# Optimization experiments

Measured on AMD Instinct MI355X. Metric: run time of the kernel, lower is better.

Reference implementation:

```python
import jax, jax.numpy as jnp
import numpy as np
from functools import partial

D_MODEL = 1024
D_STATE = 16
D_CONV = 4
EXPAND = 2
DIM = EXPAND * D_MODEL  # 2048


def setup_inputs() -> dict:
    key = jax.random.key(0)
    ks = jax.random.split(key, 10)
    s = lambda fan_in: 1.0 / np.sqrt(fan_in)
    inp = {
        "x": jax.random.normal(ks[0], (8, 2048, D_MODEL), dtype=jnp.float32),
        "W_in": jax.random.normal(ks[1], (DIM, D_MODEL), dtype=jnp.float32) * s(D_MODEL),
        "b_in": jnp.zeros((DIM,), dtype=jnp.float32),
        "conv_w": jax.random.normal(ks[2], (DIM, 1, D_CONV), dtype=jnp.float32) * s(D_CONV),
        "conv_b": jnp.zeros((DIM,), dtype=jnp.float32),
        "W_x": jax.random.normal(ks[3], (3 * D_STATE, DIM), dtype=jnp.float32) * s(DIM),
        "W_dt": jax.random.normal(ks[4], (DIM, D_STATE), dtype=jnp.float32) * s(D_STATE),
        "b_dt": jnp.zeros((DIM,), dtype=jnp.float32),
        "W_out": jax.random.normal(ks[5], (D_MODEL, DIM), dtype=jnp.float32) * s(DIM),
        "b_out": jnp.zeros((D_MODEL,), dtype=jnp.float32),
    }
    return inp


def _selective_scan(xc, delta, A, Bm, Cm):
    # xc, delta: (B, L, DIM); Bm, Cm: (B, L, N); A: (N,)
    Bsz = xc.shape[0]
    h0 = jnp.zeros((Bsz, DIM, D_STATE), dtype=xc.dtype)

    def step(h, inputs):
        xc_t, d_t, b_t, c_t = inputs  # (B,DIM),(B,DIM),(B,N),(B,N)
        h = h * jnp.exp(d_t[:, :, None] * A) + xc_t[:, :, None] * b_t[:, None, :]
        y_t = jnp.einsum("bdn,bn->bd", h, c_t)
        return h, y_t

    tm = lambda a: jnp.swapaxes(a, 0, 1)  # time-major
    _, ys = jax.lax.scan(step, h0, (tm(xc), tm(delta), tm(Bm), tm(Cm)))
    return jnp.swapaxes(ys, 0, 1)  # (B, L, DIM)


def reference(x, W_in, b_in, conv_w, conv_b, W_x, W_dt, b_dt, W_out, b_out):
    A = -jnp.exp(jnp.linspace(0.0, -5.0, D_STATE).astype(x.dtype))  # (N,)
    xp = x @ W_in.T + b_in  # (B, L, DIM)
    # depthwise conv1d, padding=D_CONV-1 on BOTH sides (as torch Conv1d) -> length L+D_CONV-1
    xc = jax.lax.conv_general_dilated(
        jnp.swapaxes(xp, 1, 2), conv_w,
        window_strides=(1,), padding=[(D_CONV - 1, D_CONV - 1)],
        feature_group_count=DIM,
        dimension_numbers=("NCH", "OIH", "NCH"),
    ) + conv_b[None, :, None]
    xc = jnp.swapaxes(xc, 1, 2)  # (B, Lc, DIM)
    x_dbl = xc @ W_x.T  # (B, Lc, 3N)
    d_raw, Bm, Cm = jnp.split(x_dbl, [D_STATE, 2 * D_STATE], axis=-1)
    delta = jax.nn.softplus(d_raw @ W_dt.T + b_dt)  # (B, Lc, DIM)
    y = _selective_scan(xc, delta, A, Bm, Cm)  # (B, Lc, DIM)
    return y @ W_out.T + b_out  # (B, Lc, D_MODEL)
```

## Files before the change

### kernel.cpp

```cpp
#include <hip/hip_runtime.h>
#include <cstdint>
#include <cstddef>

#define B8 8
#define LSEQ 2048
#define LC 2051
#define DMODEL 1024
#define DIM 2048
#define LPAD 2054
#define M2 16408
#define M2P 16512
#define CS 32
#define NCH 65

typedef __attribute__((ext_vector_type(8))) short short8;
typedef __attribute__((ext_vector_type(4))) float floatx4;
typedef __attribute__((ext_vector_type(2))) float float2v;

__device__ __constant__ float AeT[16] = {
  -1.0f,          -0.71653131f, -0.51341712f, -0.36787944f,
  -0.26359714f,   -0.18887560f, -0.13533528f, -0.09697208f,
  -0.06948345f,   -0.04978707f, -0.03567399f, -0.02556154f,
  -0.01831564f,   -0.01312373f, -0.00940356f, -0.00673795f};

#define LOG2E 1.44269504088896f

__device__ __forceinline__ float bf2f(unsigned short h) {
  union { unsigned int u; float f; } v; v.u = ((unsigned int)h) << 16; return v.f;
}
__device__ __forceinline__ unsigned short f2bf(float f) {
  union { float f; unsigned int u; } v; v.f = f;
  unsigned int r = (v.u + 0x7FFFu + ((v.u >> 16) & 1u)) >> 16;
  return (unsigned short)r;
}

__device__ __forceinline__ float2v pk_mul_vv(float2v a, float2v b) {
  float2v d; asm("v_pk_mul_f32 %0, %1, %2" : "=v"(d) : "v"(a), "v"(b)); return d;
}
__device__ __forceinline__ float2v pk_mul_sv(float2v bs, float2v a) {
  float2v d; asm("v_pk_mul_f32 %0, %1, %2" : "=v"(d) : "s"(bs), "v"(a)); return d;
}
__device__ __forceinline__ float2v pk_fma_vvv(float2v a, float2v b, float2v c) {
  float2v d; asm("v_pk_fma_f32 %0, %1, %2, %3" : "=v"(d) : "v"(a), "v"(b), "v"(c)); return d;
}
__device__ __forceinline__ float2v pk_fma_vsv(float2v a, float2v bs, float2v c) {
  float2v d; asm("v_pk_fma_f32 %0, %1, %2, %3" : "=v"(d) : "v"(a), "s"(bs), "v"(c)); return d;
}
__device__ __forceinline__ float2v pk_add_vv(float2v a, float2v b) {
  float2v d; asm("v_pk_add_f32 %0, %1, %2" : "=v"(d) : "v"(a), "v"(b)); return d;
}
__device__ __forceinline__ float exp2_raw(float x) {
  float d; asm("v_exp_f32 %0, %1" : "=v"(d) : "v"(x)); return d;
}

__global__ __launch_bounds__(256) void cvt_f32_bf16(const float* __restrict__ in,
                                                    unsigned short* __restrict__ out,
                                                    int n8) {
  int i = blockIdx.x * 256 + threadIdx.x;
  if (i >= n8) return;
  const float4* p = (const float4*)in + (size_t)i * 2;
  float4 a = p[0], b = p[1];
  uint4 o;
  o.x = (unsigned)f2bf(a.x) | ((unsigned)f2bf(a.y) << 16);
  o.y = (unsigned)f2bf(a.z) | ((unsigned)f2bf(a.w) << 16);
  o.z = (unsigned)f2bf(b.x) | ((unsigned)f2bf(b.y) << 16);
  o.w = (unsigned)f2bf(b.z) | ((unsigned)f2bf(b.w) << 16);
  *((uint4*)out + i) = o;
}

__global__ __launch_bounds__(256) void zero_pads(unsigned short* __restrict__ xp) {
  int i = blockIdx.x * 256 + threadIdx.x;
  int b = i / 1536;
  int r6 = (i % 1536) / 256;
  int dd = (i % 256) * 8;
  int row = (r6 < 3) ? r6 : (2048 + r6);
  uint4 z = make_uint4(0, 0, 0, 0);
  *(uint4*)(xp + ((size_t)b * LPAD + row) * DIM + dd) = z;
}

__global__ __launch_bounds__(256) void conv_kernel(const unsigned short* __restrict__ xp,
                                                   const float* __restrict__ conv_w,
                                                   const float* __restrict__ conv_b,
                                                   unsigned short* __restrict__ xc) {
  const int tc0 = blockIdx.x * 16;
  const int b = blockIdx.y;
  const int d0 = threadIdx.x * 8;

  float4 cw[8];
#pragma unroll
  for (int j = 0; j < 8; ++j) cw[j] = *(const float4*)(conv_w + (size_t)(d0 + j) * 4);
  float cb[8];
  {
    const float4* cb4 = (const float4*)(conv_b + d0);
    float4 c0 = cb4[0], c1 = cb4[1];
    cb[0] = c0.x; cb[1] = c0.y; cb[2] = c0.z; cb[3] = c0.w;
    cb[4] = c1.x; cb[5] = c1.y; cb[6] = c1.z; cb[7] = c1.w;
  }

  const unsigned short* base = xp + ((size_t)b * LPAD + tc0) * DIM + d0;
  unsigned short* outp = xc + ((size_t)b * LC + tc0) * DIM + d0;

  auto loadrow = [&](float (&w)[8], int r) {
    uint4 v = *(const uint4*)(base + (size_t)r * DIM);
    w[0] = bf2f(v.x & 0xffff); w[1] = bf2f(v.x >> 16);
    w[2] = bf2f(v.y & 0xffff); w[3] = bf2f(v.y >> 16);
    w[4] = bf2f(v.z & 0xffff); w[5] = bf2f(v.z >> 16);
    w[6] = bf2f(v.w & 0xffff); w[7] = bf2f(v.w >> 16);
  };

  float wa[8], wb[8], wc[8];
  loadrow(wa, 0); loadrow(wb, 1); loadrow(wc, 2);
#pragma unroll
  for (int i = 0; i < 16; ++i) {
    float wd[8];
    loadrow(wd, i + 3);
    if (tc0 + i < LC) {
      float acc[8];
#pragma unroll
      for (int j = 0; j < 8; ++j) {
        acc[j] = cb[j];
        acc[j] = fmaf(wa[j], cw[j].x, acc[j]);
        acc[j] = fmaf(wb[j], cw[j].y, acc[j]);
        acc[j] = fmaf(wc[j], cw[j].z, acc[j]);
        acc[j] = fmaf(wd[j], cw[j].w, acc[j]);
      }
      uint4 o;
      o.x = (unsigned)f2bf(acc[0]) | ((unsigned)f2bf(acc[1]) << 16);
      o.y = (unsigned)f2bf(acc[2]) | ((unsigned)f2bf(acc[3]) << 16);
      o.z = (unsigned)f2bf(acc[4]) | ((unsigned)f2bf(acc[5]) << 16);
      o.w = (unsigned)f2bf(acc[6]) | ((unsigned)f2bf(acc[7]) << 16);
      *(uint4*)(outp + (size_t)i * DIM) = o;
    }
#pragma unroll
    for (int j = 0; j < 8; ++j) { wa[j] = wb[j]; wb[j] = wc[j]; wc[j] = wd[j]; }
  }
}

#define GAS(p) ((const __attribute__((address_space(1))) void*)(p))
#define LAS(p) ((__attribute__((address_space(3))) void*)(p))

template <int MODE, int NBM, int NBN, int LX, int TAIL>
__global__ __launch_bounds__(256) void gemm_bt(const unsigned short* __restrict__ A,
                                               const unsigned short* __restrict__ Bw,
                                               const float* __restrict__ bias,
                                               void* __restrict__ Cout, int K) {
  const int gid = blockIdx.x;
  const int mainBlocks = 8 * LX * NBN;
  int bm, bn;
  if (TAIL && gid >= mainBlocks) {
    const int e = gid - mainBlocks;
    bm = 8 * LX + e / NBN;
    bn = e % NBN;
  } else {
    const int xcd = gid & 7;
    const int j = gid >> 3;
    bm = xcd * LX + (j % LX);
    bn = j / LX;
  }
  if (bm >= NBM) return;

  __shared__ __align__(16) unsigned short As[128 * 64];
  __shared__ __align__(16) unsigned short Bs[128 * 64];
  const int tid = threadIdx.x;
  const int lane = tid & 63, wave = tid >> 6;
  const int wr = wave >> 1, wc = wave & 1;

  floatx4 acc[4][4];
#pragma unroll
  for (int i = 0; i < 4; ++i)
#pragma unroll
    for (int j2 = 0; j2 < 4; ++j2) acc[i][j2] = (floatx4){0.f, 0.f, 0.f, 0.f};

  const int srow = tid >> 3;
  const int scol = ((tid & 7) ^ ((tid >> 3) & 7)) * 8;
  const unsigned short* Ab[4];
  const unsigned short* Bb[4];
#pragma unroll
  for (int L = 0; L < 4; ++L) {
    Ab[L] = A  + (size_t)(bm * 128 + L * 32 + srow) * K + scol;
    Bb[L] = Bw + (size_t)(bn * 128 + L * 32 + srow) * K + scol;
  }

  const int fr = lane & 15;
  const int hi = lane >> 4;
  const int fx = fr & 7;

  for (int k0 = 0; k0 < K; k0 += 64) {
    __syncthreads();
#pragma unroll
    for (int L = 0; L < 4; ++L) {
      __builtin_amdgcn_global_load_lds(GAS(Ab[L] + k0), LAS(As + L * 2048 + tid * 8), 16, 0, 0);
      __builtin_amdgcn_global_load_lds(GAS(Bb[L] + k0), LAS(Bs + L * 2048 + tid * 8), 16, 0, 0);
    }
    __syncthreads();

#pragma unroll
    for (int kk = 0; kk < 2; ++kk) {
      const int pb = ((kk * 4 + hi) ^ fx) * 8;
      short8 af[4], bf[4];
#pragma unroll
      for (int mt = 0; mt < 4; ++mt) af[mt] = *(const short8*)&As[(wr * 64 + mt * 16 + fr) * 64 + pb];
#pragma unroll
      for (int nt = 0; nt < 4; ++nt) bf[nt] = *(const short8*)&Bs[(wc * 64 + nt * 16 + fr) * 64 + pb];
#pragma unroll
      for (int mt = 0; mt < 4; ++mt)
#pragma unroll
        for (int nt = 0; nt < 4; ++nt)
          acc[mt][nt] = __builtin_amdgcn_mfma_f32_16x16x32_bf16(af[mt], bf[nt], acc[mt][nt], 0, 0, 0);
    }
  }

  const int er = (lane >> 4) * 4, ec = lane & 15;
#pragma unroll
  for (int mt = 0; mt < 4; ++mt) {
#pragma unroll
    for (int nt = 0; nt < 4; ++nt) {
#pragma unroll
      for (int i = 0; i < 4; ++i) {
        int r = bm * 128 + wr * 64 + mt * 16 + er + i;
        int c = bn * 128 + wc * 64 + nt * 16 + ec;
        float v = acc[mt][nt][i];
        if constexpr (MODE == 0) {
          int bb = r >> 11, t = r & 2047;
          ((unsigned short*)Cout)[((size_t)bb * LPAD + 3 + t) * DIM + c] = f2bf(v + bias[c]);
        } else if constexpr (MODE == 1) {
          if (r < M2 && c < 48) ((float*)Cout)[(size_t)r * 48 + c] = v;
        } else {
          if (r < M2) ((float*)Cout)[(size_t)r * DMODEL + c] = v + bias[c];
        }
      }
    }
  }
}

__global__ __launch_bounds__(256) void delta_kernel(const float* __restrict__ xdbl,
                                                    const float* __restrict__ W_dt,
                                                    const float* __restrict__ b_dt,
                                                    unsigned short* __restrict__ delta) {
  const int d = blockIdx.y * 256 + threadIdx.x;
  const int r0 = blockIdx.x * 8;
  float wv[16];
  const float4* wp = (const float4*)(W_dt + (size_t)d * 16);
#pragma unroll
  for (int q = 0; q < 4; ++q) {
    float4 t = wp[q];
    wv[q * 4 + 0] = t.x; wv[q * 4 + 1] = t.y; wv[q * 4 + 2] = t.z; wv[q * 4 + 3] = t.w;
  }
  const float bd = b_dt[d];
#pragma unroll
  for (int j = 0; j < 8; ++j) {
    const float* dr = xdbl + (size_t)(r0 + j) * 48;
    float z0 = bd, z1 = 0.f, z2 = 0.f, z3 = 0.f;
#pragma unroll
    for (int n = 0; n < 16; n += 4) {
      z0 = fmaf(dr[n + 0], wv[n + 0], z0);
      z1 = fmaf(dr[n + 1], wv[n + 1], z1);
      z2 = fmaf(dr[n + 2], wv[n + 2], z2);
      z3 = fmaf(dr[n + 3], wv[n + 3], z3);
    }
    float z = (z0 + z1) + (z2 + z3);
    float dl = (z > 20.f) ? z : __logf(1.f + __expf(z));
    delta[(size_t)(r0 + j) * DIM + d] = f2bf(dl);
  }
}

__global__ __launch_bounds__(256) void scan_pass1(const unsigned short* __restrict__ xc,
                                                  const unsigned short* __restrict__ dl,
                                                  const float* __restrict__ xd,
                                                  unsigned short* __restrict__ sdbuf,
                                                  unsigned short* __restrict__ qbuf) {
  const int wid = __builtin_amdgcn_readfirstlane((int)(threadIdx.x >> 6));
  const int lane = threadIdx.x & 63;
  const int W = blockIdx.x * 4 + wid;
  const int dg = W & 31;
  const int rest = W >> 5;
  const int c = rest % NCH;
  const int b = rest / NCH;
  const int d = dg * 64 + lane;
  const int t0 = c * CS;
  const int nst = (t0 + CS <= LC) ? CS : (LC - t0);

  float2v A2L[8];
#pragma unroll
  for (int i = 0; i < 8; ++i)
    A2L[i] = (float2v){AeT[2 * i] * LOG2E, AeT[2 * i + 1] * LOG2E};

  float2v h2[8];
#pragma unroll
  for (int i = 0; i < 8; ++i) h2[i] = (float2v){0.f, 0.f};
  float sumd = 0.f;

  const size_t row0 = (size_t)b * LC + t0;
  const float* xdb = xd + row0 * 48 + 16;
  const unsigned short* xcp = xc + row0 * DIM + d;
  const unsigned short* dp  = dl + row0 * DIM + d;

  auto body = [&](int s) {
    float2v Bv[8];
#pragma unroll
    for (int j = 0; j < 8; ++j) Bv[j] = *(const float2v*)(xdb + (size_t)s * 48 + 2 * j);
    float dlt = bf2f(dp[(size_t)s * DIM]);
    float xcv = bf2f(xcp[(size_t)s * DIM]);
    sumd += dlt;
    float2v dlt2 = (float2v){dlt, dlt};
    float2v xcv2 = (float2v){xcv, xcv};
#pragma unroll
    for (int i = 0; i < 8; ++i) {
      float2v arg = pk_mul_vv(dlt2, A2L[i]);
      float e0 = exp2_raw(arg.x), e1 = exp2_raw(arg.y);
      float2v e2 = (float2v){e0, e1};
      h2[i] = pk_fma_vvv(h2[i], e2, pk_mul_sv(Bv[i], xcv2));
    }
  };

  if (nst == CS) {
#pragma unroll
    for (int s = 0; s < CS; ++s) body(s);
  } else {
    for (int s = 0; s < nst; ++s) body(s);
  }

  sdbuf[((size_t)(b * NCH + c) << 11) + d] = f2bf(sumd);
  const size_t base = ((size_t)(b * NCH + c) * 16) * 2048 + d;
#pragma unroll
  for (int i = 0; i < 8; ++i) {
    qbuf[base + ((size_t)(2 * i) << 11)]     = f2bf(h2[i].x);
    qbuf[base + ((size_t)(2 * i + 1) << 11)] = f2bf(h2[i].y);
  }
}

__global__ __launch_bounds__(256) void scan_boundary(const unsigned short* __restrict__ sdbuf,
                                                     unsigned short* __restrict__ qbuf) {
  const int tid = threadIdx.x;
  const int n = tid >> 4;
  const int d = blockIdx.x * 16 + (tid & 15);
  const int b = blockIdx.y;
  const float aL = AeT[n] * LOG2E;
  float h = 0.f;
  for (int c = 0; c < NCH; ++c) {
    const size_t sbase = ((size_t)(b * NCH + c) << 11);
    const float sd = bf2f(sdbuf[sbase + d]);
    const size_t base = (sbase << 4) + ((size_t)n << 11) + d;
    const float qv = bf2f(qbuf[base]);
    const float Pv = exp2_raw(sd * aL);
    qbuf[base] = f2bf(h);
    h = fmaf(Pv, h, qv);
  }
}

__global__ __launch_bounds__(256) void scan_pass2(const unsigned short* __restrict__ xc,
                                                  const unsigned short* __restrict__ dl,
                                                  const float* __restrict__ xd,
                                                  const unsigned short* __restrict__ hinit,
                                                  unsigned short* __restrict__ y) {
  const int wid = __builtin_amdgcn_readfirstlane((int)(threadIdx.x >> 6));
  const int lane = threadIdx.x & 63;
  const int W = blockIdx.x * 4 + wid;
  const int dg = W & 31;
  const int rest = W >> 5;
  const int c = rest % NCH;
  const int b = rest / NCH;
  const int d = dg * 64 + lane;
  const int t0 = c * CS;
  const int nst = (t0 + CS <= LC) ? CS : (LC - t0);

  float2v A2L[8];
#pragma unroll
  for (int i = 0; i < 8; ++i)
    A2L[i] = (float2v){AeT[2 * i] * LOG2E, AeT[2 * i + 1] * LOG2E};

  const size_t base = ((size_t)(b * NCH + c) * 16) * 2048 + d;
  float2v h2[8];
#pragma unroll
  for (int i = 0; i < 8; ++i)
    h2[i] = (float2v){bf2f(hinit[base + ((size_t)(2 * i) << 11)]),
                      bf2f(hinit[base + ((size_t)(2 * i + 1) << 11)])};

  const size_t row0 = (size_t)b * LC + t0;
  const float* xdb = xd + row0 * 48 + 16;
  const unsigned short* xcp = xc + row0 * DIM + d;
  const unsigned short* dp  = dl + row0 * DIM + d;
  unsigned short* yp = y + row0 * DIM + d;

  auto body = [&](int s) {
    float2v Bv[8], Cv[8];
#pragma unroll
    for (int j = 0; j < 8; ++j) {
      Bv[j] = *(const float2v*)(xdb + (size_t)s * 48 + 2 * j);
      Cv[j] = *(const float2v*)(xdb + (size_t)s * 48 + 16 + 2 * j);
    }
    float dlt = bf2f(dp[(size_t)s * DIM]);
    float xcv = bf2f(xcp[(size_t)s * DIM]);
    float2v dlt2 = (float2v){dlt, dlt};
    float2v xcv2 = (float2v){xcv, xcv};
    float2v y2[4];
#pragma unroll
    for (int i = 0; i < 4; ++i) y2[i] = (float2v){0.f, 0.f};
#pragma unroll
    for (int i = 0; i < 8; ++i) {
      float2v arg = pk_mul_vv(dlt2, A2L[i]);
      float e0 = exp2_raw(arg.x), e1 = exp2_raw(arg.y);
      float2v e2 = (float2v){e0, e1};
      h2[i] = pk_fma_vvv(h2[i], e2, pk_mul_sv(Bv[i], xcv2));
      y2[i & 3] = pk_fma_vsv(h2[i], Cv[i], y2[i & 3]);
    }
    float2v s01 = pk_add_vv(y2[0], y2[1]);
    float2v s23 = pk_add_vv(y2[2], y2[3]);
    float2v st = pk_add_vv(s01, s23);
    yp[(size_t)s * DIM] = f2bf(st.x + st.y);
  };

  if (nst == CS) {
#pragma unroll
    for (int s = 0; s < CS; ++s) body(s);
  } else {
    for (int s = 0; s < nst; ++s) body(s);
  }
}

extern "C" void kernel_launch(void* const* d_in, const int* in_sizes, int n_in,
                              void* d_out, int out_size, void* d_ws, size_t ws_size,
                              hipStream_t stream) {
  const float* x      = (const float*)d_in[0];
  const float* W_in   = (const float*)d_in[1];
  const float* b_in   = (const float*)d_in[2];
  const float* conv_w = (const float*)d_in[3];
  const float* conv_b = (const float*)d_in[4];
  const float* W_x    = (const float*)d_in[5];
  const float* W_dt   = (const float*)d_in[6];
  const float* b_dt   = (const float*)d_in[7];
  const float* W_out  = (const float*)d_in[8];
  const float* b_out  = (const float*)d_in[9];

  char* w = (char*)d_ws;
  unsigned short* xp    = (unsigned short*)w;
  unsigned short* delta = (unsigned short*)w;
  unsigned short* ybuf  = (unsigned short*)w;
  size_t off = (size_t)M2P * DIM * 2;
  unsigned short* xcb  = (unsigned short*)(w + off); off += (size_t)M2P * DIM * 2;
  size_t xA_off = off;
  unsigned short* xA   = (unsigned short*)(w + off); off += (size_t)16384 * 1024 * 2;
  unsigned short* wInB = (unsigned short*)(w + off); off += (size_t)2048 * 1024 * 2;
  unsigned short* wOutB= (unsigned short*)(w + off); off += (size_t)1024 * 2048 * 2;
  unsigned short* wXB  = (unsigned short*)(w + off); off += (size_t)128 * 2048 * 2;
  float* xdbl          = (float*)(w + off);          off += (size_t)M2 * 48 * 4;
  unsigned short* sdbuf = (unsigned short*)(w + xA_off);
  unsigned short* qbuf  = (unsigned short*)(w + xA_off + (size_t)B8 * NCH * 2048 * 2);
  (void)ws_size; (void)in_sizes; (void)n_in; (void)out_size;

  cvt_f32_bf16<<<8192, 256, 0, stream>>>(x, xA, 2097152);
  cvt_f32_bf16<<<1024, 256, 0, stream>>>(W_in, wInB, 262144);
  cvt_f32_bf16<<<1024, 256, 0, stream>>>(W_out, wOutB, 262144);
  cvt_f32_bf16<<<48,   256, 0, stream>>>(W_x, wXB, 12288);
  zero_pads<<<48, 256, 0, stream>>>(xp);

  gemm_bt<0, 128, 16, 16, 0><<<2048, 256, 0, stream>>>(xA, wInB, b_in, xp, 1024);
  conv_kernel<<<dim3(129, B8), 256, 0, stream>>>(xp, conv_w, conv_b, xcb);
  gemm_bt<1, 129, 1, 16, 1><<<129, 256, 0, stream>>>(xcb, wXB, nullptr, xdbl, 2048);
  delta_kernel<<<dim3(2051, 8), 256, 0, stream>>>(xdbl, W_dt, b_dt, delta);

  scan_pass1<<<4160, 256, 0, stream>>>(xcb, delta, xdbl, sdbuf, qbuf);
  scan_boundary<<<dim3(128, B8), 256, 0, stream>>>(sdbuf, qbuf);
  scan_pass2<<<4160, 256, 0, stream>>>(xcb, delta, xdbl, qbuf, ybuf);

  gemm_bt<2, 129, 8, 16, 1><<<1032, 256, 0, stream>>>(ybuf, wOutB, b_out, (float*)d_out, 2048);
}
```

Baseline: 537.7 us.

## Double-buffer GEMM LDS tiles and merge conversion/pad-zeroing launches into one kernel

The bf16 GEMM now keeps two LDS buffers and issues the global-to-LDS load for the next K tile before computing the current one, so memory latency overlaps with MFMA work. It also switches to explicit ds_read_b128 loads and raises wave priority around the MFMA block. Separately, the four dtype-conversion launches and the pad-zeroing launch are merged into a single init kernel to cut launch overhead. Doubling the LDS footprint to 64KB per block may lower occupancy, and the waitcnt and sync placement has to be correct for the async LDS loads.

```diff
diff --git a/kernel.cpp b/kernel.cpp
--- a/kernel.cpp
+++ b/kernel.cpp
@@ -16,6 +16,7 @@
 typedef __attribute__((ext_vector_type(8))) short short8;
 typedef __attribute__((ext_vector_type(4))) float floatx4;
 typedef __attribute__((ext_vector_type(2))) float float2v;
+typedef __attribute__((address_space(3))) unsigned short lds_ushort;
 
 __device__ __constant__ float AeT[16] = {
   -1.0f,          -0.71653131f, -0.51341712f, -0.36787944f,
@@ -53,11 +54,37 @@
   float d; asm("v_exp_f32 %0, %1" : "=v"(d) : "v"(x)); return d;
 }
 
-__global__ __launch_bounds__(256) void cvt_f32_bf16(const float* __restrict__ in,
-                                                    unsigned short* __restrict__ out,
-                                                    int n8) {
-  int i = blockIdx.x * 256 + threadIdx.x;
-  if (i >= n8) return;
+__device__ __forceinline__ short8 ds_read_b128_(const lds_ushort* p) {
+  floatx4 d;
+  unsigned addr = (unsigned)(size_t)p;
+  asm volatile("ds_read_b128 %0, %1" : "=v"(d) : "v"(addr));
+  return __builtin_bit_cast(short8, d);
+}
+
+__global__ __launch_bounds__(256) void init_kernel(const float* __restrict__ x,
+                                                   const float* __restrict__ W_in,
+                                                   const float* __restrict__ W_out,
+                                                   const float* __restrict__ W_x,
+                                                   unsigned short* __restrict__ xA,
+                                                   unsigned short* __restrict__ wInB,
+                                                   unsigned short* __restrict__ wOutB,
+                                                   unsigned short* __restrict__ wXB,
+                                                   unsigned short* __restrict__ xp) {
+  const int gid = blockIdx.x;
+  const float* in; unsigned short* out; int i;
+  if (gid < 8192)        { in = x;     out = xA;    i = gid * 256 + threadIdx.x; }
+  else if (gid < 9216)   { in = W_in;  out = wInB;  i = (gid - 8192) * 256 + threadIdx.x; }
+  else if (gid < 10240)  { in = W_out; out = wOutB; i = (gid - 9216) * 256 + threadIdx.x; }
+  else if (gid < 10288)  { in = W_x;   out = wXB;   i = (gid - 10240) * 256 + threadIdx.x; }
+  else {
+    int ii = (gid - 10288) * 256 + threadIdx.x;
+    int b = ii / 1536;
+    int r6 = (ii % 1536) / 256;
+    int dd = (ii % 256) * 8;
+    int row = (r6 < 3) ? r6 : (2048 + r6);
+    *(uint4*)(xp + ((size_t)b * LPAD + row) * DIM + dd) = make_uint4(0, 0, 0, 0);
+    return;
+  }
   const float4* p = (const float4*)in + (size_t)i * 2;
   float4 a = p[0], b = p[1];
   uint4 o;
@@ -66,16 +93,6 @@
   o.z = (unsigned)f2bf(b.x) | ((unsigned)f2bf(b.y) << 16);
   o.w = (unsigned)f2bf(b.z) | ((unsigned)f2bf(b.w) << 16);
   *((uint4*)out + i) = o;
-}
-
-__global__ __launch_bounds__(256) void zero_pads(unsigned short* __restrict__ xp) {
-  int i = blockIdx.x * 256 + threadIdx.x;
-  int b = i / 1536;
-  int r6 = (i % 1536) / 256;
-  int dd = (i % 256) * 8;
-  int row = (r6 < 3) ? r6 : (2048 + r6);
-  uint4 z = make_uint4(0, 0, 0, 0);
-  *(uint4*)(xp + ((size_t)b * LPAD + row) * DIM + dd) = z;
 }
 
 __global__ __launch_bounds__(256) void conv_kernel(const unsigned short* __restrict__ xp,
@@ -159,8 +176,8 @@
   }
   if (bm >= NBM) return;
 
-  __shared__ __align__(16) unsigned short As[128 * 64];
-  __shared__ __align__(16) unsigned short Bs[128 * 64];
+  __shared__ __align__(16) unsigned short As[2][128 * 64];
+  __shared__ __align__(16) unsigned short Bs[2][128 * 64];
   const int tid = threadIdx.x;
   const int lane = tid & 63, wave = tid >> 6;
   const int wr = wave >> 1, wc = wave & 1;
@@ -185,29 +202,45 @@
   const int hi = lane >> 4;
   const int fx = fr & 7;
 
-  for (int k0 = 0; k0 < K; k0 += 64) {
-    __syncthreads();
+  auto STAGE = [&](int buf, int k0) {
 #pragma unroll
     for (int L = 0; L < 4; ++L) {
-      __builtin_amdgcn_global_load_lds(GAS(Ab[L] + k0), LAS(As + L * 2048 + tid * 8), 16, 0, 0);
-      __builtin_amdgcn_global_load_lds(GAS(Bb[L] + k0), LAS(Bs + L * 2048 + tid * 8), 16, 0, 0);
-    }
-    __syncthreads();
-
+      __builtin_amdgcn_global_load_lds(GAS(Ab[L] + k0), LAS(&As[buf][L * 2048 + tid * 8]), 16, 0, 0);
+      __builtin_amdgcn_global_load_lds(GAS(Bb[L] + k0), LAS(&Bs[buf][L * 2048 + tid * 8]), 16, 0, 0);
+    }
+  };
+
+  const int NT = K >> 6;
+  STAGE(0, 0);
+  asm volatile("s_waitcnt vmcnt(0)");
+  __syncthreads();
+
+  int cur = 0;
+  for (int t = 0; t < NT; ++t) {
+    if (t + 1 < NT) STAGE(cur ^ 1, (t + 1) * 64);
+
+    const lds_ushort* tA = (const lds_ushort*)LAS(&As[cur][0]);
+    const lds_ushort* tB = (const lds_ushort*)LAS(&Bs[cur][0]);
 #pragma unroll
     for (int kk = 0; kk < 2; ++kk) {
       const int pb = ((kk * 4 + hi) ^ fx) * 8;
       short8 af[4], bf[4];
 #pragma unroll
-      for (int mt = 0; mt < 4; ++mt) af[mt] = *(const short8*)&As[(wr * 64 + mt * 16 + fr) * 64 + pb];
-#pragma unroll
-      for (int nt = 0; nt < 4; ++nt) bf[nt] = *(const short8*)&Bs[(wc * 64 + nt * 16 + fr) * 64 + pb];
+      for (int mt = 0; mt < 4; ++mt) af[mt] = ds_read_b128_(tA + (wr * 64 + mt * 16 + fr) * 64 + pb);
+#pragma unroll
+      for (int nt = 0; nt < 4; ++nt) bf[nt] = ds_read_b128_(tB + (wc * 64 + nt * 16 + fr) * 64 + pb);
+      asm volatile("s_waitcnt lgkmcnt(0)");
+      __builtin_amdgcn_sched_barrier(0);
+      __builtin_amdgcn_s_setprio(1);
 #pragma unroll
       for (int mt = 0; mt < 4; ++mt)
 #pragma unroll
         for (int nt = 0; nt < 4; ++nt)
           acc[mt][nt] = __builtin_amdgcn_mfma_f32_16x16x32_bf16(af[mt], bf[nt], acc[mt][nt], 0, 0, 0);
-    }
+      __builtin_amdgcn_s_setprio(0);
+    }
+    __syncthreads();
+    cur ^= 1;
   }
 
   const int er = (lane >> 4) * 4, ec = lane & 15;
@@ -448,11 +481,7 @@
   unsigned short* qbuf  = (unsigned short*)(w + xA_off + (size_t)B8 * NCH * 2048 * 2);
   (void)ws_size; (void)in_sizes; (void)n_in; (void)out_size;
 
-  cvt_f32_bf16<<<8192, 256, 0, stream>>>(x, xA, 2097152);
-  cvt_f32_bf16<<<1024, 256, 0, stream>>>(W_in, wInB, 262144);
-  cvt_f32_bf16<<<1024, 256, 0, stream>>>(W_out, wOutB, 262144);
-  cvt_f32_bf16<<<48,   256, 0, stream>>>(W_x, wXB, 12288);
-  zero_pads<<<48, 256, 0, stream>>>(xp);
+  init_kernel<<<10336, 256, 0, stream>>>(x, W_in, W_out, W_x, xA, wInB, wOutB, wXB, xp);
 
   gemm_bt<0, 128, 16, 16, 0><<<2048, 256, 0, stream>>>(xA, wInB, b_in, xp, 1024);
   conv_kernel<<<dim3(129, B8), 256, 0, stream>>>(xp, conv_w, conv_b, xcb);
```

New measurement: 521.2 us. 3.1% less time.
